# Kernel optimization log

Hardware: AMD Instinct MI355X
Metric: run time of the kernel (lower is better)

Reference implementation:

```python
import jax, jax.numpy as jnp
import numpy as np

N_NODES = 8192
N_EDGES = 131072  # avg degree 16
SD = 64   # state_dim == message_dim (required by readout input size)
MD = 64
H = 128   # hidden_unit_message_dim
HR = 128  # hidden_unit_readout_dim


def setup_inputs() -> dict:
    rng = np.random.default_rng(0)
    # distinct nonzero positions of J (COO), emulating torch.nonzero(J)
    flat = rng.choice(N_NODES * N_NODES, size=N_EDGES, replace=False)
    row = jnp.asarray(flat // N_NODES, dtype=jnp.int32)
    col = jnp.asarray(flat % N_NODES, dtype=jnp.int32)
    jvals = jnp.asarray(rng.normal(size=N_EDGES).astype(np.float32))  # J[row, col]
    b = jnp.asarray(rng.normal(size=N_NODES).astype(np.float32))     # unused by forward (as in source)

    key = jax.random.key(0)
    ks = jax.random.split(key, 12)
    p = lambda k, shape: 0.1 * jax.random.normal(k, shape, dtype=jnp.float32)
    return dict(
        jvals=jvals, b=b, row=row, col=col,
        conv_W=p(ks[0], (2, H, H)),          # GatedGraphConv per-layer weight
        gru_wi=p(ks[1], (3 * H, H)),          # GRUCell input weights (torch layout [3h,h])
        gru_wh=p(ks[2], (3 * H, H)),
        gru_bi=jnp.zeros((3 * H,), jnp.float32),
        gru_bh=jnp.zeros((3 * H,), jnp.float32),
        mp_W1=p(ks[3], (H, H)),  mp_b1=jnp.zeros((H,), jnp.float32),
        mp_W2=p(ks[4], (H, H)),  mp_b2=jnp.zeros((H,), jnp.float32),
        mp_W3=p(ks[5], (H, MD)), mp_b3=jnp.zeros((MD,), jnp.float32),
        ro_W1=p(ks[6], (SD, HR)), ro_b1=jnp.zeros((HR,), jnp.float32),
        ro_W2=p(ks[7], (HR, HR)), ro_b2=jnp.zeros((HR,), jnp.float32),
        ro_W3=p(ks[8], (HR, 2)),  ro_b3=jnp.zeros((2,), jnp.float32),
    )


def _ggnn_forward(jvals, b, row, col, conv_W, gru_wi, gru_wh, gru_bi, gru_bh,
                  mp_W1, mp_b1, mp_W2, mp_b2, mp_W3, mp_b3,
                  ro_W1, ro_b1, ro_W2, ro_b2, ro_W3, ro_b3):
    n_nodes = b.shape[0]
    n_edges = row.shape[0]
    n_tot = n_nodes + n_edges  # variable nodes + factor nodes

    # initial node states padded to hidden dim H (GatedGraphConv zero-pads input)
    x = jnp.zeros((n_tot, H), dtype=jvals.dtype)
    x = x.at[n_nodes:, 0].set(1.0).at[n_nodes:, 1].set(jvals)

    # bipartite factor-graph edges: factor e <-> row[e], factor e <-> col[e]
    fac = n_nodes + jnp.arange(n_edges, dtype=row.dtype)
    src = jnp.concatenate([fac, row, fac, col])
    dst = jnp.concatenate([row, fac, col, fac])

    # GatedGraphConv: 2 layers of (linear -> add-aggregate -> GRUCell)
    for l in range(2):
        m = x @ conv_W[l]                                   # [n_tot, H]
        agg = jax.ops.segment_sum(m[src], dst, num_segments=n_tot)
        gi = agg @ gru_wi.T + gru_bi                        # [n_tot, 3H]
        gh = x @ gru_wh.T + gru_bh
        i_r, i_z, i_n = jnp.split(gi, 3, axis=1)
        h_r, h_z, h_n = jnp.split(gh, 3, axis=1)
        r = jax.nn.sigmoid(i_r + h_r)
        z = jax.nn.sigmoid(i_z + h_z)
        n = jnp.tanh(i_n + r * h_n)
        x = (1.0 - z) * n + z * x

    # message MLP on factor-node states -> per-edge messages [n_edges, MD]
    xf = x[n_nodes:]
    hm = jax.nn.relu(xf @ mp_W1 + mp_b1)
    hm = jax.nn.relu(hm @ mp_W2 + mp_b2)
    msgs = hm @ mp_W3 + mp_b3

    # Special3dSpmm with b = ones: per-dim sparse row sums == segment_sum by row
    node_msgs = jax.ops.segment_sum(msgs, row, num_segments=n_nodes)  # [n_nodes, MD]

    hr = jax.nn.relu(node_msgs @ ro_W1 + ro_b1)
    hr = jax.nn.relu(hr @ ro_W2 + ro_b2)
    logits = hr @ ro_W3 + ro_b3
    return jax.nn.softmax(logits, axis=1)  # [n_nodes, 2]


def reference(jvals, b, row, col, conv_W, gru_wi, gru_wh, gru_bi, gru_bh,
              mp_W1, mp_b1, mp_W2, mp_b2, mp_W3, mp_b3,
              ro_W1, ro_b1, ro_W2, ro_b2, ro_W3, ro_b3):
    return _ggnn_forward(jvals, b, row, col, conv_W, gru_wi, gru_wh, gru_bi, gru_bh,
                         mp_W1, mp_b1, mp_W2, mp_b2, mp_W3, mp_b3,
                         ro_W1, ro_b1, ro_W2, ro_b2, ro_W3, ro_b3)
```

## Files before the change

### kernel.cpp

```cpp
#include <hip/hip_runtime.h>
#include <hip/hip_bf16.h>
#include <cstdint>

#define N_NODES 8192
#define N_EDGES 131072
#define NTOT 139264
#define H 128

typedef __attribute__((ext_vector_type(8))) short short8;
typedef __attribute__((ext_vector_type(4))) float floatx4;

__device__ __forceinline__ ushort f2bf(float f) {
    union { float f; uint32_t u; } v; v.f = f;
    uint32_t r = v.u + 0x7fffu + ((v.u >> 16) & 1u);
    return (ushort)(r >> 16);
}
__device__ __forceinline__ float bf2f(ushort u) {
    union { uint32_t u; float f; } v; v.u = ((uint32_t)u) << 16;
    return v.f;
}
__device__ __forceinline__ float bflo(uint u) { union { uint32_t u; float f; } v; v.u = u << 16; return v.f; }
__device__ __forceinline__ float bfhi(uint u) { union { uint32_t u; float f; } v; v.u = u & 0xffff0000u; return v.f; }
__device__ __forceinline__ uint packbf(float a, float b) { return (uint)f2bf(a) | ((uint)f2bf(b) << 16); }

__device__ __forceinline__ float fsig(float x) { return __builtin_amdgcn_rcpf(1.f + __expf(-x)); }
__device__ __forceinline__ float ftanh(float x) { return fmaf(2.f, fsig(2.f * x), -1.f); }

__device__ __forceinline__ short8 lds_load8(const ushort* p) {
    union { short8 s; uint2 u[2]; } r;
    r.u[0] = *(const uint2*)p;
    r.u[1] = *(const uint2*)(p + 4);
    return r.s;
}
__device__ __forceinline__ short8 glb_load8(const ushort* p) {
    union { short8 s; uint4 u; } r;
    r.u = *(const uint4*)p;
    return r.s;
}
__device__ __forceinline__ floatx4 mfma16(short8 a, short8 b, floatx4 c) {
    return __builtin_amdgcn_mfma_f32_16x16x32_bf16(a, b, c, 0, 0, 0);
}

__global__ __launch_bounds__(256) void k_setup(
    const float* __restrict__ convW, const float* __restrict__ wi, const float* __restrict__ wh,
    const float* __restrict__ m1, const float* __restrict__ m2, const float* __restrict__ m3,
    const float* __restrict__ r1, const float* __restrict__ r2,
    ushort* __restrict__ W, ushort* __restrict__ Wci,
    float* __restrict__ wh01, float* __restrict__ wci01)
{
    int idx = blockIdx.x * 256 + threadIdx.x;
    if (idx < 196608) {
        if (idx < 32768) { W[idx] = 0; return; }
        float v;
        if (idx < 81920)       v = wi[idx - 32768];
        else if (idx < 131072) v = wh[idx - 81920];
        else if (idx < 147456) { int t = idx - 131072; int n = t >> 7, k = t & 127; v = m1[k * 128 + n]; }
        else if (idx < 163840) { int t = idx - 147456; int n = t >> 7, k = t & 127; v = m2[k * 128 + n]; }
        else if (idx < 172032) { int t = idx - 163840; int n = t >> 7, k = t & 127; v = m3[k * 64 + n];  }
        else if (idx < 180224) { int t = idx - 172032; int n = t >> 6, k = t & 63;  v = r1[k * 128 + n]; }
        else                   { int t = idx - 180224; int n = t >> 7, k = t & 127; v = r2[k * 128 + n]; }
        W[idx] = f2bf(v);
    } else if (idx < 245760) {
        int t = idx - 196608;
        int n = t >> 7, k = t & 127;
        const float* wc = convW + 16384 + k * 128;
        const float* wr = wi + n * 128;
        float s = 0.f;
        #pragma unroll 8
        for (int j = 0; j < 128; ++j) s = fmaf(wc[j], wr[j], s);
        Wci[t] = f2bf(s);
    } else if (idx < 246528) {
        int n = idx - 245760;
        wh01[n] = wh[(n >> 1) * 128 + (n & 1)];
    } else if (idx < 247296) {
        int m = idx - 246528;
        int c = m >> 1, wsel = m & 1;
        const float* wc = convW + wsel * 128;
        const float* wr = wi + c * 128;
        float s = 0.f;
        #pragma unroll 8
        for (int j = 0; j < 128; ++j) s = fmaf(wc[j], wr[j], s);
        wci01[m] = s;
    }
}

__global__ __launch_bounds__(256) void k_zero_deg(int* __restrict__ deg, int* __restrict__ deg2) {
    int i = blockIdx.x * 256 + threadIdx.x;
    if (i < 8192) { deg[i] = 0; deg2[i] = 0; }
}

__global__ __launch_bounds__(256) void k_deg_count(const int* __restrict__ row, const int* __restrict__ col,
                                                   int* __restrict__ deg, int* __restrict__ deg2) {
    int e = blockIdx.x * 256 + threadIdx.x;
    atomicAdd(&deg[row[e]], 1);
    atomicAdd(&deg[col[e]], 1);
    atomicAdd(&deg2[row[e]], 1);
}

__global__ __launch_bounds__(256) void k_scan(const int* __restrict__ deg, int* __restrict__ start, int* __restrict__ cur,
                                              const int* __restrict__ deg2, int* __restrict__ start2, int* __restrict__ cur2) {
    __shared__ int s1[256], s2[256];
    int tid = threadIdx.x, base = tid * 32;
    int a = 0, b = 0;
    for (int i = 0; i < 32; ++i) { a += deg[base + i]; b += deg2[base + i]; }
    s1[tid] = a; s2[tid] = b;
    __syncthreads();
    if (tid == 0) {
        int acc = 0, acc2 = 0;
        for (int i = 0; i < 256; ++i) {
            int t = s1[i]; s1[i] = acc; acc += t;
            int u = s2[i]; s2[i] = acc2; acc2 += u;
        }
    }
    __syncthreads();
    int off = s1[tid], off2 = s2[tid];
    for (int i = 0; i < 32; ++i) {
        start[base + i] = off;  cur[base + i] = off;   off += deg[base + i];
        start2[base + i] = off2; cur2[base + i] = off2; off2 += deg2[base + i];
    }
}

__global__ __launch_bounds__(256) void k_fill(const int* __restrict__ row, const int* __restrict__ col,
                                              int* __restrict__ cur, int* __restrict__ cur2,
                                              int* __restrict__ list, int* __restrict__ list2) {
    int e = blockIdx.x * 256 + threadIdx.x;
    int p = atomicAdd(&cur[row[e]], 1);  list[p] = e;
    int q = atomicAdd(&cur[col[e]], 1);  list[q] = e;
    int r2 = atomicAdd(&cur2[row[e]], 1); list2[r2] = e;
}

#define SORT_BUF 256
__global__ __launch_bounds__(256) void k_sort(
    const int* __restrict__ start, const int* __restrict__ deg,
    const int* __restrict__ start2, const int* __restrict__ deg2,
    int* __restrict__ list, int* __restrict__ list2,
    const float* __restrict__ jvals, float* __restrict__ sj)
{
    __shared__ int bufU[4][SORT_BUF];
    __shared__ int bufS[4][SORT_BUF];
    const int wv = threadIdx.x >> 6, lane = threadIdx.x & 63;
    const int task = blockIdx.x * 4 + wv;
    const bool second = task >= 8192;
    const int node = second ? task - 8192 : task;
    const int s = second ? start2[node] : start[node];
    const int d = second ? deg2[node] : deg[node];
    int* L = second ? list2 : list;
    int* BU = bufU[wv];
    int* BS = bufS[wv];

    for (int i = lane; i < d && i < SORT_BUF; i += 64) BU[i] = L[s + i];
    __syncthreads();
    if (d <= SORT_BUF) {
        for (int i = lane; i < d; i += 64) {
            int v = BU[i];
            int rank = 0;
            for (int j = 0; j < d; ++j)
                rank += (BU[j] < v) || (BU[j] == v && j < i);
            L[s + rank] = v;
            BS[rank] = v;
        }
    } else if (lane == 0) {
        for (int a = 1; a < d; ++a) {
            int v = L[s + a]; int b = a - 1;
            while (b >= 0 && L[s + b] > v) { L[s + b + 1] = L[s + b]; --b; }
            L[s + b + 1] = v;
        }
    }
    __syncthreads();
    if (!second) {
        float a = 0.f;
        if (d <= SORT_BUF) {
            for (int i = lane; i < d; i += 64) a += jvals[BS[i]];
        } else if (lane == 0) {
            for (int i = 0; i < d; ++i) a += jvals[L[s + i]];
        }
        for (int off = 32; off; off >>= 1) a += __shfl_down(a, off);
        if (lane == 0) sj[node] = a;
    }
}

__global__ __launch_bounds__(256) void k_l1_fac(
    const float* __restrict__ jvals, const float* __restrict__ wh01,
    const float* __restrict__ bi, const float* __restrict__ bh, ushort* __restrict__ X1)
{
    int idx = blockIdx.x * 256 + threadIdx.x;
    int e = idx >> 6, cp = idx & 63;
    float jv = jvals[e];
    float res[2];
    #pragma unroll
    for (int t = 0; t < 2; ++t) {
        int c = 2 * cp + t;
        float ghr = fmaf(jv, wh01[c * 2 + 1], wh01[c * 2]) + bh[c];
        float ghz = fmaf(jv, wh01[(128 + c) * 2 + 1], wh01[(128 + c) * 2]) + bh[128 + c];
        float ghn = fmaf(jv, wh01[(256 + c) * 2 + 1], wh01[(256 + c) * 2]) + bh[256 + c];
        float r = fsig(bi[c] + ghr);
        float z = fsig(bi[128 + c] + ghz);
        float nn = ftanh(fmaf(r, ghn, bi[256 + c]));
        float x0 = (c == 0) ? 1.f : (c == 1 ? jv : 0.f);
        res[t] = (1.f - z) * nn + z * x0;
    }
    *(uint*)(X1 + (size_t)(N_NODES + e) * H + 2 * cp) = packbf(res[0], res[1]);
}

__global__ __launch_bounds__(256) void k_l1_nodes(
    const int* __restrict__ deg, const float* __restrict__ sj, const float* __restrict__ wci01,
    const float* __restrict__ bi, const float* __restrict__ bh, ushort* __restrict__ X1)
{
    int idx = blockIdx.x * 256 + threadIdx.x;
    int n = idx >> 6, cp = idx & 63;
    float d = (float)deg[n], s = sj[n];
    float res[2];
    #pragma unroll
    for (int t = 0; t < 2; ++t) {
        int c = 2 * cp + t;
        float gir = fmaf(s, wci01[c * 2 + 1], fmaf(d, wci01[c * 2], bi[c]));
        float giz = fmaf(s, wci01[(128 + c) * 2 + 1], fmaf(d, wci01[(128 + c) * 2], bi[128 + c]));
        float gin = fmaf(s, wci01[(256 + c) * 2 + 1], fmaf(d, wci01[(256 + c) * 2], bi[256 + c]));
        float r = fsig(gir + bh[c]);
        float z = fsig(giz + bh[128 + c]);
        float nn = ftanh(fmaf(r, bh[256 + c], gin));
        res[t] = (1.f - z) * nn;
    }
    *(uint*)(X1 + (size_t)n * H + 2 * cp) = packbf(res[0], res[1]);
}

__global__ __launch_bounds__(256) void k_agg_nodes(uint* __restrict__ Pn, const uint* __restrict__ X,
                                                   const int* __restrict__ start, const int* __restrict__ deg,
                                                   const int* __restrict__ list) {
    int node = blockIdx.x * 4 + (threadIdx.x >> 6);
    int lane = threadIdx.x & 63;
    int s = start[node], d = deg[node];
    float a0 = 0.f, b0 = 0.f, a1 = 0.f, b1 = 0.f;
    int i = 0;
    for (; i + 1 < d; i += 2) {
        uint v0 = X[(size_t)(N_NODES + list[s + i]) * 64 + lane];
        uint v1 = X[(size_t)(N_NODES + list[s + i + 1]) * 64 + lane];
        a0 += bflo(v0); b0 += bfhi(v0);
        a1 += bflo(v1); b1 += bfhi(v1);
    }
    if (i < d) {
        uint v0 = X[(size_t)(N_NODES + list[s + i]) * 64 + lane];
        a0 += bflo(v0); b0 += bfhi(v0);
    }
    Pn[(size_t)node * 64 + lane] = packbf(a0 + a1, b0 + b1);
}

__global__ __launch_bounds__(256) void k_nm_gather(float* __restrict__ nm, const ushort* __restrict__ msgs,
                                                   const int* __restrict__ start2, const int* __restrict__ deg2,
                                                   const int* __restrict__ list2) {
    int node = blockIdx.x * 4 + (threadIdx.x >> 6);
    int lane = threadIdx.x & 63;
    int s = start2[node], d = deg2[node];
    float a0 = 0.f, a1 = 0.f;
    int i = 0;
    for (; i + 1 < d; i += 2) {
        a0 += bf2f(msgs[(size_t)list2[s + i] * 64 + lane]);
        a1 += bf2f(msgs[(size_t)list2[s + i + 1] * 64 + lane]);
    }
    if (i < d) a0 += bf2f(msgs[(size_t)list2[s + i] * 64 + lane]);
    nm[(size_t)node * 64 + lane] = a0 + a1;
}

__global__ __launch_bounds__(256) void k_logits(const ushort* __restrict__ hr2, const float* __restrict__ W3,
                                                const float* __restrict__ b3, float* __restrict__ out) {
    int r = blockIdx.x * 4 + (threadIdx.x >> 6);
    int lane = threadIdx.x & 63;
    float l0 = 0.f, l1 = 0.f;
    for (int k = lane; k < H; k += 64) {
        float hv = bf2f(hr2[(size_t)r * H + k]);
        l0 = fmaf(hv, W3[k * 2 + 0], l0);
        l1 = fmaf(hv, W3[k * 2 + 1], l1);
    }
    for (int off = 32; off; off >>= 1) { l0 += __shfl_down(l0, off); l1 += __shfl_down(l1, off); }
    if (lane == 0) {
        l0 += b3[0]; l1 += b3[1];
        float mx = fmaxf(l0, l1);
        float e0 = __expf(l0 - mx), e1 = __expf(l1 - mx), s = e0 + e1;
        out[r * 2 + 0] = e0 / s;
        out[r * 2 + 1] = e1 / s;
    }
}

template<int BN, bool AF32, bool RELU, bool OUTF32>
__global__ __launch_bounds__(256) void k_gemm2(
    const void* __restrict__ Aptr, const ushort* __restrict__ Bt,
    const float* __restrict__ bias, void* __restrict__ Cptr, int K, int lda)
{
    constexpr int BM = 128, LK = 136;
    constexpr int MI = (BN == 128) ? 4 : 2;
    constexpr int NI = 4;
    __shared__ ushort As[BM * LK];
    __shared__ ushort Bs[BN * LK];
    const int tid = threadIdx.x;
    const size_t row0 = (size_t)blockIdx.x * BM;
    const int kpc = K >> 3;

    if (AF32) {
        const float* A = (const float*)Aptr;
        for (int id = tid; id < BM * kpc; id += 256) {
            int m = id / kpc, kc = id - m * kpc;
            float4 v0 = *(const float4*)(A + (row0 + m) * lda + kc * 8);
            float4 v1 = *(const float4*)(A + (row0 + m) * lda + kc * 8 + 4);
            uint4 u;
            u.x = packbf(v0.x, v0.y); u.y = packbf(v0.z, v0.w);
            u.z = packbf(v1.x, v1.y); u.w = packbf(v1.z, v1.w);
            *(uint4*)&As[m * LK + kc * 8] = u;
        }
    } else {
        const ushort* A = (const ushort*)Aptr;
        for (int id = tid; id < BM * kpc; id += 256) {
            int m = id / kpc, kc = id - m * kpc;
            *(uint4*)&As[m * LK + kc * 8] = *(const uint4*)(A + (row0 + m) * (size_t)lda + kc * 8);
        }
    }
    for (int id = tid; id < BN * kpc; id += 256) {
        int slot = id / kpc, kc = id - slot * kpc;
        int gcol = (slot & ~63) + 4 * (slot & 15) + ((slot >> 4) & 3);
        *(uint4*)&Bs[slot * LK + kc * 8] = *(const uint4*)(Bt + (size_t)gcol * K + kc * 8);
    }
    __syncthreads();

    const int w = tid >> 6, lane = tid & 63, quad = lane >> 4, l15 = lane & 15;
    const int wr = (BN == 128) ? (w >> 1) * 64 : w * 32;
    const int wc = (BN == 128) ? (w & 1) * 64 : 0;

    floatx4 acc[MI][NI];
    #pragma unroll
    for (int i = 0; i < MI; ++i)
        #pragma unroll
        for (int j = 0; j < NI; ++j) acc[i][j] = (floatx4)0.f;

    for (int k0 = 0; k0 < K; k0 += 32) {
        short8 a[MI], b[NI];
        #pragma unroll
        for (int mi = 0; mi < MI; ++mi) a[mi] = lds_load8(&As[(wr + mi * 16 + l15) * LK + k0 + quad * 8]);
        #pragma unroll
        for (int ni = 0; ni < NI; ++ni) b[ni] = lds_load8(&Bs[(wc + ni * 16 + l15) * LK + k0 + quad * 8]);
        #pragma unroll
        for (int mi = 0; mi < MI; ++mi)
            #pragma unroll
            for (int ni = 0; ni < NI; ++ni)
                acc[mi][ni] = mfma16(a[mi], b[ni], acc[mi][ni]);
    }

    float bv[NI];
    #pragma unroll
    for (int ni = 0; ni < NI; ++ni) bv[ni] = bias ? bias[wc + 4 * l15 + ni] : 0.f;
    #pragma unroll
    for (int mi = 0; mi < MI; ++mi) {
        #pragma unroll
        for (int reg = 0; reg < 4; ++reg) {
            size_t r = row0 + wr + mi * 16 + quad * 4 + reg;
            float v[NI];
            #pragma unroll
            for (int ni = 0; ni < NI; ++ni) {
                v[ni] = acc[mi][ni][reg] + bv[ni];
                if (RELU) v[ni] = fmaxf(v[ni], 0.f);
            }
            if (OUTF32) {
                float4 o = make_float4(v[0], v[1], v[2], v[3]);
                *(float4*)((float*)Cptr + r * BN + wc + 4 * l15) = o;
            } else {
                uint2 o = make_uint2(packbf(v[0], v[1]), packbf(v[2], v[3]));
                *(uint2*)((ushort*)Cptr + r * BN + wc + 4 * l15) = o;
            }
        }
    }
}

__global__ __launch_bounds__(512, 4) void k_gru6(
    const ushort* __restrict__ Pn, const ushort* __restrict__ Xin, ushort* __restrict__ Xout,
    const int* __restrict__ row, const int* __restrict__ col,
    const ushort* __restrict__ WCI, const ushort* __restrict__ WH,
    const float* __restrict__ bi, const float* __restrict__ bh)
{
    constexpr int LK = 136;
    __shared__ ushort Ws[3 * 64 * LK];
    const int tid = threadIdx.x;
    const int c0 = blockIdx.x * 64;
    const size_t brow0 = (size_t)blockIdx.y * 128;
    const bool isFac = blockIdx.y >= (N_NODES / 128);
    const int w = tid >> 6, lane = tid & 63, quad = lane >> 4, l15 = lane & 15;
    const int ch = w & 1;
    const size_t row0 = brow0 + (w >> 1) * 32;
    const int cb = c0 + ch * 32;

    int srcR[2], srcC[2];
    if (isFac) {
        #pragma unroll
        for (int mi = 0; mi < 2; ++mi) {
            int e = (int)(row0 + mi * 16 + l15) - N_NODES;
            srcR[mi] = row[e];
            srcC[mi] = col[e];
        }
    }

    floatx4 accR[2][2], accZ[2][2], accI[2][2], accHN[2][2];
    #pragma unroll
    for (int i = 0; i < 2; ++i)
        #pragma unroll
        for (int j = 0; j < 2; ++j) {
            accR[i][j] = (floatx4)0.f; accZ[i][j] = (floatx4)0.f;
            accI[i][j] = (floatx4)0.f; accHN[i][j] = (floatx4)0.f;
        }

    #pragma unroll
    for (int h = 0; h < 2; ++h) {
        if (h) __syncthreads();
        const ushort* Wsrc = h ? WH : WCI;
        for (int id = tid; id < 3072; id += 512) {
            int kc = id & 15, slot = (id >> 4) & 63, s = id >> 10;
            int w32 = slot & 31;
            int gcol = c0 + (slot >> 5) * 32 + 2 * (w32 & 15) + (w32 >> 4);
            *(uint4*)&Ws[(s * 64 + slot) * LK + kc * 8] =
                *(const uint4*)(Wsrc + (size_t)(s * 128 + gcol) * 128 + kc * 8);
        }
        __syncthreads();
        if (h == 0) {
            if (isFac) {
                #pragma unroll
                for (int k4 = 0; k4 < 4; ++k4) {
                    const int k0 = k4 * 32;
                    short8 ar[2], ac[2];
                    #pragma unroll
                    for (int mi = 0; mi < 2; ++mi) {
                        ar[mi] = glb_load8(Xin + (size_t)srcR[mi] * H + k0 + quad * 8);
                        ac[mi] = glb_load8(Xin + (size_t)srcC[mi] * H + k0 + quad * 8);
                    }
                    #pragma unroll
                    for (int s = 0; s < 3; ++s) {
                        short8 b[2];
                        #pragma unroll
                        for (int ni = 0; ni < 2; ++ni)
                            b[ni] = lds_load8(&Ws[(s * 64 + ch * 32 + ni * 16 + l15) * LK + k0 + quad * 8]);
                        #pragma unroll
                        for (int mi = 0; mi < 2; ++mi)
                            #pragma unroll
                            for (int ni = 0; ni < 2; ++ni) {
                                if (s == 0) { accR[mi][ni] = mfma16(ar[mi], b[ni], accR[mi][ni]);
                                              accR[mi][ni] = mfma16(ac[mi], b[ni], accR[mi][ni]); }
                                else if (s == 1) { accZ[mi][ni] = mfma16(ar[mi], b[ni], accZ[mi][ni]);
                                                   accZ[mi][ni] = mfma16(ac[mi], b[ni], accZ[mi][ni]); }
                                else { accI[mi][ni] = mfma16(ar[mi], b[ni], accI[mi][ni]);
                                       accI[mi][ni] = mfma16(ac[mi], b[ni], accI[mi][ni]); }
                            }
                    }
                }
            } else {
                #pragma unroll
                for (int k4 = 0; k4 < 4; ++k4) {
                    const int k0 = k4 * 32;
                    short8 a[2];
                    #pragma unroll
                    for (int mi = 0; mi < 2; ++mi)
                        a[mi] = glb_load8(Pn + (row0 + mi * 16 + l15) * H + k0 + quad * 8);
                    #pragma unroll
                    for (int s = 0; s < 3; ++s) {
                        short8 b[2];
                        #pragma unroll
                        for (int ni = 0; ni < 2; ++ni)
                            b[ni] = lds_load8(&Ws[(s * 64 + ch * 32 + ni * 16 + l15) * LK + k0 + quad * 8]);
                        #pragma unroll
                        for (int mi = 0; mi < 2; ++mi)
                            #pragma unroll
                            for (int ni = 0; ni < 2; ++ni) {
                                if (s == 0)      accR[mi][ni] = mfma16(a[mi], b[ni], accR[mi][ni]);
                                else if (s == 1) accZ[mi][ni] = mfma16(a[mi], b[ni], accZ[mi][ni]);
                                else             accI[mi][ni] = mfma16(a[mi], b[ni], accI[mi][ni]);
                            }
                    }
                }
            }
        } else {
            #pragma unroll
            for (int k4 = 0; k4 < 4; ++k4) {
                const int k0 = k4 * 32;
                short8 a[2];
                #pragma unroll
                for (int mi = 0; mi < 2; ++mi)
                    a[mi] = glb_load8(Xin + (row0 + mi * 16 + l15) * H + k0 + quad * 8);
                #pragma unroll
                for (int s = 0; s < 3; ++s) {
                    short8 b[2];
                    #pragma unroll
                    for (int ni = 0; ni < 2; ++ni)
                        b[ni] = lds_load8(&Ws[(s * 64 + ch * 32 + ni * 16 + l15) * LK + k0 + quad * 8]);
                    #pragma unroll
                    for (int mi = 0; mi < 2; ++mi)
                        #pragma unroll
                        for (int ni = 0; ni < 2; ++ni) {
                            if (s == 0)      accR[mi][ni] = mfma16(a[mi], b[ni], accR[mi][ni]);
                            else if (s == 1) accZ[mi][ni] = mfma16(a[mi], b[ni], accZ[mi][ni]);
                            else             accHN[mi][ni] = mfma16(a[mi], b[ni], accHN[mi][ni]);
                        }
                }
            }
        }
    }

    const int ce = cb + 2 * l15;
    float bir[2], biz[2], bin_[2], bhr[2], bhz[2], bhn[2];
    #pragma unroll
    for (int ni = 0; ni < 2; ++ni) {
        bir[ni] = bi[ce + ni]; biz[ni] = bi[128 + ce + ni]; bin_[ni] = bi[256 + ce + ni];
        bhr[ni] = bh[ce + ni]; bhz[ni] = bh[128 + ce + ni]; bhn[ni] = bh[256 + ce + ni];
    }
    #pragma unroll
    for (int mi = 0; mi < 2; ++mi)
        #pragma unroll
        for (int reg = 0; reg < 4; ++reg) {
            size_t r = row0 + mi * 16 + quad * 4 + reg;
            uint xo = *(const uint*)(Xin + r * H + ce);
            float xold[2] = { bflo(xo), bfhi(xo) };
            float res[2];
            #pragma unroll
            for (int ni = 0; ni < 2; ++ni) {
                float rs = accR[mi][ni][reg] + bir[ni] + bhr[ni];
                float zs = accZ[mi][ni][reg] + biz[ni] + bhz[ni];
                float rr = fsig(rs);
                float zz = fsig(zs);
                float nn = ftanh(accI[mi][ni][reg] + bin_[ni] + rr * (accHN[mi][ni][reg] + bhn[ni]));
                res[ni] = (1.f - zz) * nn + zz * xold[ni];
            }
            *(uint*)(Xout + r * H + ce) = packbf(res[0], res[1]);
        }
}

__global__ __launch_bounds__(256, 3) void k_mlp(
    const ushort* __restrict__ Xf, const ushort* __restrict__ W1, const ushort* __restrict__ W2,
    const ushort* __restrict__ W3, const float* __restrict__ b1, const float* __restrict__ b2,
    const float* __restrict__ b3, ushort* __restrict__ msgs)
{
    constexpr int LK = 132;
    __shared__ ushort T[128 * LK];
    __shared__ ushort Wv[64 * LK];
    const int tid = threadIdx.x;
    const size_t row0 = (size_t)blockIdx.x * 128;
    const int w = tid >> 6, lane = tid & 63, quad = lane >> 4, l15 = lane & 15;
    const int wr = w * 32;

    for (int id = tid; id < 2048; id += 256) {
        int m = id >> 4, kc = (id & 15) * 8;
        *(uint4*)&T[m * LK + kc] = *(const uint4*)(Xf + (row0 + m) * H + kc);
    }

    #pragma unroll
    for (int stage = 0; stage < 3; ++stage) {
        const ushort* Wsrc = (stage == 0) ? W1 : (stage == 1) ? W2 : W3;
        const float* bias = (stage == 0) ? b1 : (stage == 1) ? b2 : b3;
        const int NCG = (stage == 2) ? 1 : 2;
        floatx4 acc[2][2][4];
        #pragma unroll
        for (int c = 0; c < 2; ++c)
            #pragma unroll
            for (int i = 0; i < 2; ++i)
                #pragma unroll
                for (int j = 0; j < 4; ++j) acc[c][i][j] = (floatx4)0.f;

        for (int cg = 0; cg < NCG; ++cg) {
            __syncthreads();
            for (int id = tid; id < 1024; id += 256) {
                int slot = id >> 4, kc = (id & 15) * 8;
                int gcol = cg * 64 + 4 * (slot & 15) + (slot >> 4);
                *(uint4*)&Wv[slot * LK + kc] = *(const uint4*)(Wsrc + (size_t)gcol * 128 + kc);
            }
            __syncthreads();
            for (int k0 = 0; k0 < 128; k0 += 32) {
                short8 a[2], b[4];
                #pragma unroll
                for (int mi = 0; mi < 2; ++mi)
                    a[mi] = lds_load8(&T[(wr + mi * 16 + l15) * LK + k0 + quad * 8]);
                #pragma unroll
                for (int ni = 0; ni < 4; ++ni)
                    b[ni] = lds_load8(&Wv[(ni * 16 + l15) * LK + k0 + quad * 8]);
                #pragma unroll
                for (int mi = 0; mi < 2; ++mi)
                    #pragma unroll
                    for (int ni = 0; ni < 4; ++ni)
                        acc[cg][mi][ni] = mfma16(a[mi], b[ni], acc[cg][mi][ni]);
            }
        }
        __syncthreads();

        if (stage < 2) {
            #pragma unroll
            for (int cg = 0; cg < 2; ++cg) {
                float bv[4];
                #pragma unroll
                for (int ni = 0; ni < 4; ++ni) bv[ni] = bias[cg * 64 + 4 * l15 + ni];
                #pragma unroll
                for (int mi = 0; mi < 2; ++mi)
                    #pragma unroll
                    for (int reg = 0; reg < 4; ++reg) {
                        int r = wr + mi * 16 + quad * 4 + reg;
                        float v[4];
                        #pragma unroll
                        for (int ni = 0; ni < 4; ++ni)
                            v[ni] = fmaxf(acc[cg][mi][ni][reg] + bv[ni], 0.f);
                        uint2 o = make_uint2(packbf(v[0], v[1]), packbf(v[2], v[3]));
                        *(uint2*)&T[r * LK + cg * 64 + 4 * l15] = o;
                    }
            }
            __syncthreads();
        } else {
            float bv[4];
            #pragma unroll
            for (int ni = 0; ni < 4; ++ni) bv[ni] = bias[4 * l15 + ni];
            #pragma unroll
            for (int mi = 0; mi < 2; ++mi)
                #pragma unroll
                for (int reg = 0; reg < 4; ++reg) {
                    size_t r = row0 + wr + mi * 16 + quad * 4 + reg;
                    float v[4];
                    #pragma unroll
                    for (int ni = 0; ni < 4; ++ni) v[ni] = acc[0][mi][ni][reg] + bv[ni];
                    uint2 o = make_uint2(packbf(v[0], v[1]), packbf(v[2], v[3]));
                    *(uint2*)(msgs + r * 64 + 4 * l15) = o;
                }
        }
    }
}

extern "C" void kernel_launch(void* const* d_in, const int* in_sizes, int n_in,
                              void* d_out, int out_size, void* d_ws, size_t ws_size,
                              hipStream_t stream) {
    (void)in_sizes; (void)n_in; (void)out_size;
    const float* jvals  = (const float*)d_in[0];
    const int*   row    = (const int*)d_in[2];
    const int*   col    = (const int*)d_in[3];
    const float* conv_W = (const float*)d_in[4];
    const float* gru_wi = (const float*)d_in[5];
    const float* gru_wh = (const float*)d_in[6];
    const float* gru_bi = (const float*)d_in[7];
    const float* gru_bh = (const float*)d_in[8];
    const float* mp_W1  = (const float*)d_in[9];
    const float* mp_b1  = (const float*)d_in[10];
    const float* mp_W2  = (const float*)d_in[11];
    const float* mp_b2  = (const float*)d_in[12];
    const float* mp_W3  = (const float*)d_in[13];
    const float* mp_b3  = (const float*)d_in[14];
    const float* ro_b1  = (const float*)d_in[16];
    const float* ro_b2  = (const float*)d_in[18];
    const float* ro_W3  = (const float*)d_in[19];
    const float* ro_b3  = (const float*)d_in[20];

    constexpr size_t OFF_XB  = 35651584ull;
    constexpr size_t OFF_P   = 71303168ull;
    constexpr size_t OFF_W   = 106954752ull;
    constexpr size_t OFF_WCI = 107347968ull;
    constexpr size_t OFF_NM  = 107544576ull;
    constexpr size_t OFF_HR1 = 109641728ull;
    constexpr size_t OFF_HR2 = 111738880ull;
    constexpr size_t OFF_CSR = 113836032ull;
    constexpr size_t OFF_L1  = 114032640ull;
    constexpr size_t OFF_L2  = 115081216ull;
    constexpr size_t OFF_SJ  = 115605504ull;
    constexpr size_t OFF_WH01  = 115638272ull;
    constexpr size_t OFF_WCI01 = 115641344ull;
    constexpr size_t WS_NEED = 115644416ull;
    if (ws_size < WS_NEED) return;

    char* ws = (char*)d_ws;
    ushort* X2   = (ushort*)ws;
    ushort* X1   = (ushort*)(ws + OFF_XB);
    ushort* Pn   = (ushort*)(ws + OFF_P);
    ushort* msgs = (ushort*)(ws + OFF_P);
    ushort* Wb   = (ushort*)(ws + OFF_W);
    ushort* Wci  = (ushort*)(ws + OFF_WCI);
    float*  nm   = (float*)(ws + OFF_NM);
    ushort* hr1  = (ushort*)(ws + OFF_HR1);
    ushort* hr2  = (ushort*)(ws + OFF_HR2);
    int* deg    = (int*)(ws + OFF_CSR);
    int* start  = deg + 8192;
    int* cur    = deg + 16384;
    int* deg2   = deg + 24576;
    int* start2 = deg + 32768;
    int* cur2   = deg + 40960;
    int* list   = (int*)(ws + OFF_L1);
    int* list2  = (int*)(ws + OFF_L2);
    float* sj    = (float*)(ws + OFF_SJ);
    float* wh01  = (float*)(ws + OFF_WH01);
    float* wci01 = (float*)(ws + OFF_WCI01);

    dim3 blk(256);

    k_setup<<<966, blk, 0, stream>>>(conv_W, gru_wi, gru_wh, mp_W1, mp_W2, mp_W3,
                                     (const float*)d_in[15], (const float*)d_in[17],
                                     Wb, Wci, wh01, wci01);
    k_zero_deg<<<32, blk, 0, stream>>>(deg, deg2);
    k_deg_count<<<N_EDGES / 256, blk, 0, stream>>>(row, col, deg, deg2);
    k_scan<<<1, blk, 0, stream>>>(deg, start, cur, deg2, start2, cur2);
    k_fill<<<N_EDGES / 256, blk, 0, stream>>>(row, col, cur, cur2, list, list2);
    k_sort<<<4096, blk, 0, stream>>>(start, deg, start2, deg2, list, list2, jvals, sj);

    k_l1_fac<<<N_EDGES * 64 / 256, blk, 0, stream>>>(jvals, wh01, gru_bi, gru_bh, X1);
    k_l1_nodes<<<N_NODES * 64 / 256, blk, 0, stream>>>(deg, sj, wci01, gru_bi, gru_bh, X1);

    k_agg_nodes<<<N_NODES / 4, blk, 0, stream>>>((uint*)Pn, (const uint*)X1, start, deg, list);
    k_gru6<<<dim3(2, NTOT / 128), dim3(512), 0, stream>>>(Pn, X1, X2, row, col,
        Wci, Wb + 81920, gru_bi, gru_bh);

    k_mlp<<<N_EDGES / 128, blk, 0, stream>>>(
        X2 + (size_t)N_NODES * H, Wb + 131072, Wb + 147456, Wb + 163840,
        mp_b1, mp_b2, mp_b3, msgs);

    k_nm_gather<<<N_NODES / 4, blk, 0, stream>>>(nm, msgs, start2, deg2, list2);

    k_gemm2<128, true, true, false><<<N_NODES / 128, blk, 0, stream>>>(
        nm, Wb + 172032, ro_b1, hr1, 64, 64);
    k_gemm2<128, false, true, false><<<N_NODES / 128, blk, 0, stream>>>(
        hr1, Wb + 180224, ro_b2, hr2, 128, 128);
    k_logits<<<N_NODES / 4, blk, 0, stream>>>(hr2, ro_W3, ro_b3, (float*)d_out);
}
```

Measured before the change: 357.3 us.

## Process both column halves per GRU block and stage output through LDS

The layer-2 GRU kernel now has each block loop over both 64-column halves of the output, instead of launching two blocks per row tile. The gathered row/col indices are loaded once per block, and the activation rows are re-read while still likely resident in cache. Results are written to a shared-memory tile first and then stored to global memory as coalesced 16-byte rows, replacing the scattered 4-byte stores. The cost is half as many blocks, more barriers, and weights reloaded into LDS four times per block instead of twice.

```diff
diff --git a/kernel.cpp b/kernel.cpp
--- a/kernel.cpp
+++ b/kernel.cpp
@@ -368,7 +368,7 @@
     }
 }
 
-__global__ __launch_bounds__(512, 4) void k_gru6(
+__global__ __launch_bounds__(512, 4) void k_gru7(
     const ushort* __restrict__ Pn, const ushort* __restrict__ Xin, ushort* __restrict__ Xout,
     const int* __restrict__ row, const int* __restrict__ col,
     const ushort* __restrict__ WCI, const ushort* __restrict__ WH,
@@ -376,14 +376,14 @@
 {
     constexpr int LK = 136;
     __shared__ ushort Ws[3 * 64 * LK];
+    uint* tile32 = (uint*)Ws;
     const int tid = threadIdx.x;
-    const int c0 = blockIdx.x * 64;
-    const size_t brow0 = (size_t)blockIdx.y * 128;
-    const bool isFac = blockIdx.y >= (N_NODES / 128);
+    const size_t brow0 = (size_t)blockIdx.x * 128;
+    const bool isFac = blockIdx.x >= (N_NODES / 128);
     const int w = tid >> 6, lane = tid & 63, quad = lane >> 4, l15 = lane & 15;
     const int ch = w & 1;
-    const size_t row0 = brow0 + (w >> 1) * 32;
-    const int cb = c0 + ch * 32;
+    const int wg = w >> 1;
+    const size_t row0 = brow0 + wg * 32;
 
     int srcR[2], srcC[2];
     if (isFac) {
@@ -395,55 +395,82 @@
         }
     }
 
-    floatx4 accR[2][2], accZ[2][2], accI[2][2], accHN[2][2];
-    #pragma unroll
-    for (int i = 0; i < 2; ++i)
-        #pragma unroll
-        for (int j = 0; j < 2; ++j) {
-            accR[i][j] = (floatx4)0.f; accZ[i][j] = (floatx4)0.f;
-            accI[i][j] = (floatx4)0.f; accHN[i][j] = (floatx4)0.f;
-        }
-
-    #pragma unroll
-    for (int h = 0; h < 2; ++h) {
-        if (h) __syncthreads();
-        const ushort* Wsrc = h ? WH : WCI;
-        for (int id = tid; id < 3072; id += 512) {
-            int kc = id & 15, slot = (id >> 4) & 63, s = id >> 10;
-            int w32 = slot & 31;
-            int gcol = c0 + (slot >> 5) * 32 + 2 * (w32 & 15) + (w32 >> 4);
-            *(uint4*)&Ws[(s * 64 + slot) * LK + kc * 8] =
-                *(const uint4*)(Wsrc + (size_t)(s * 128 + gcol) * 128 + kc * 8);
-        }
-        __syncthreads();
-        if (h == 0) {
-            if (isFac) {
-                #pragma unroll
-                for (int k4 = 0; k4 < 4; ++k4) {
-                    const int k0 = k4 * 32;
-                    short8 ar[2], ac[2];
+    for (int p = 0; p < 2; ++p) {
+        const int c0 = p * 64;
+        floatx4 accR[2][2], accZ[2][2], accI[2][2], accHN[2][2];
+        #pragma unroll
+        for (int i = 0; i < 2; ++i)
+            #pragma unroll
+            for (int j = 0; j < 2; ++j) {
+                accR[i][j] = (floatx4)0.f; accZ[i][j] = (floatx4)0.f;
+                accI[i][j] = (floatx4)0.f; accHN[i][j] = (floatx4)0.f;
+            }
+
+        #pragma unroll
+        for (int h = 0; h < 2; ++h) {
+            __syncthreads();
+            const ushort* Wsrc = h ? WH : WCI;
+            for (int id = tid; id < 3072; id += 512) {
+                int kc = id & 15, slot = (id >> 4) & 63, s = id >> 10;
+                int w32 = slot & 31;
+                int gcol = c0 + (slot >> 5) * 32 + 2 * (w32 & 15) + (w32 >> 4);
+                *(uint4*)&Ws[(s * 64 + slot) * LK + kc * 8] =
+                    *(const uint4*)(Wsrc + (size_t)(s * 128 + gcol) * 128 + kc * 8);
+            }
+            __syncthreads();
+            if (h == 0) {
+                if (isFac) {
                     #pragma unroll
-                    for (int mi = 0; mi < 2; ++mi) {
-                        ar[mi] = glb_load8(Xin + (size_t)srcR[mi] * H + k0 + quad * 8);
-                        ac[mi] = glb_load8(Xin + (size_t)srcC[mi] * H + k0 + quad * 8);
+                    for (int k4 = 0; k4 < 4; ++k4) {
+                        const int k0 = k4 * 32;
+                        short8 ar[2], ac[2];
+                        #pragma unroll
+                        for (int mi = 0; mi < 2; ++mi) {
+                            ar[mi] = glb_load8(Xin + (size_t)srcR[mi] * H + k0 + quad * 8);
+                            ac[mi] = glb_load8(Xin + (size_t)srcC[mi] * H + k0 + quad * 8);
+                        }
+                        #pragma unroll
+                        for (int s = 0; s < 3; ++s) {
+                            short8 b[2];
+                            #pragma unroll
+                            for (int ni = 0; ni < 2; ++ni)
+                                b[ni] = lds_load8(&Ws[(s * 64 + ch * 32 + ni * 16 + l15) * LK + k0 + quad * 8]);
+                            #pragma unroll
+                            for (int mi = 0; mi < 2; ++mi)
+                                #pragma unroll
+                                for (int ni = 0; ni < 2; ++ni) {
+                                    if (s == 0) { accR[mi][ni] = mfma16(ar[mi], b[ni], accR[mi][ni]);
+                                                  accR[mi][ni] = mfma16(ac[mi], b[ni], accR[mi][ni]); }
+                                    else if (s == 1) { accZ[mi][ni] = mfma16(ar[mi], b[ni], accZ[mi][ni]);
+                                                       accZ[mi][ni] = mfma16(ac[mi], b[ni], accZ[mi][ni]); }
+                                    else { accI[mi][ni] = mfma16(ar[mi], b[ni], accI[mi][ni]);
+                                           accI[mi][ni] = mfma16(ac[mi], b[ni], accI[mi][ni]); }
+                                }
+                        }
                     }
+                } else {
                     #pragma unroll
-                    for (int s = 0; s < 3; ++s) {
-                        short8 b[2];
-                        #pragma unroll
-                        for (int ni = 0; ni < 2; ++ni)
-                            b[ni] = lds_load8(&Ws[(s * 64 + ch * 32 + ni * 16 + l15) * LK + k0 + quad * 8]);
+                    for (int k4 = 0; k4 < 4; ++k4) {
+                        const int k0 = k4 * 32;
+                        short8 a[2];
                         #pragma unroll
                         for (int mi = 0; mi < 2; ++mi)
+                            a[mi] = glb_load8(Pn + (row0 + mi * 16 + l15) * H + k0 + quad * 8);
+                        #pragma unroll
+                        for (int s = 0; s < 3; ++s) {
+                            short8 b[2];
                             #pragma unroll
-                            for (int ni = 0; ni < 2; ++ni) {
-                                if (s == 0) { accR[mi][ni] = mfma16(ar[mi], b[ni], accR[mi][ni]);
-                                              accR[mi][ni] = mfma16(ac[mi], b[ni], accR[mi][ni]); }
-                                else if (s == 1) { accZ[mi][ni] = mfma16(ar[mi], b[ni], accZ[mi][ni]);
-                                                   accZ[mi][ni] = mfma16(ac[mi], b[ni], accZ[mi][ni]); }
-                                else { accI[mi][ni] = mfma16(ar[mi], b[ni], accI[mi][ni]);
-                                       accI[mi][ni] = mfma16(ac[mi], b[ni], accI[mi][ni]); }
-                            }
+                            for (int ni = 0; ni < 2; ++ni)
+                                b[ni] = lds_load8(&Ws[(s * 64 + ch * 32 + ni * 16 + l15) * LK + k0 + quad * 8]);
+                            #pragma unroll
+                            for (int mi = 0; mi < 2; ++mi)
+                                #pragma unroll
+                                for (int ni = 0; ni < 2; ++ni) {
+                                    if (s == 0)      accR[mi][ni] = mfma16(a[mi], b[ni], accR[mi][ni]);
+                                    else if (s == 1) accZ[mi][ni] = mfma16(a[mi], b[ni], accZ[mi][ni]);
+                                    else             accI[mi][ni] = mfma16(a[mi], b[ni], accI[mi][ni]);
+                                }
+                        }
                     }
                 }
             } else {
@@ -453,7 +480,7 @@
                     short8 a[2];
                     #pragma unroll
                     for (int mi = 0; mi < 2; ++mi)
-                        a[mi] = glb_load8(Pn + (row0 + mi * 16 + l15) * H + k0 + quad * 8);
+                        a[mi] = glb_load8(Xin + (row0 + mi * 16 + l15) * H + k0 + quad * 8);
                     #pragma unroll
                     for (int s = 0; s < 3; ++s) {
                         short8 b[2];
@@ -466,64 +493,56 @@
                             for (int ni = 0; ni < 2; ++ni) {
                                 if (s == 0)      accR[mi][ni] = mfma16(a[mi], b[ni], accR[mi][ni]);
                                 else if (s == 1) accZ[mi][ni] = mfma16(a[mi], b[ni], accZ[mi][ni]);
-                                else             accI[mi][ni] = mfma16(a[mi], b[ni], accI[mi][ni]);
+                                else             accHN[mi][ni] = mfma16(a[mi], b[ni], accHN[mi][ni]);
                             }
                     }
                 }
             }
-        } else {
-            #pragma unroll
-            for (int k4 = 0; k4 < 4; ++k4) {
-                const int k0 = k4 * 32;
-                short8 a[2];
-                #pragma unroll
-                for (int mi = 0; mi < 2; ++mi)
-                    a[mi] = glb_load8(Xin + (row0 + mi * 16 + l15) * H + k0 + quad * 8);
-                #pragma unroll
-                for (int s = 0; s < 3; ++s) {
-                    short8 b[2];
-                    #pragma unroll
-                    for (int ni = 0; ni < 2; ++ni)
-                        b[ni] = lds_load8(&Ws[(s * 64 + ch * 32 + ni * 16 + l15) * LK + k0 + quad * 8]);
-                    #pragma unroll
-                    for (int mi = 0; mi < 2; ++mi)
-                        #pragma unroll
-                        for (int ni = 0; ni < 2; ++ni) {
-                            if (s == 0)      accR[mi][ni] = mfma16(a[mi], b[ni], accR[mi][ni]);
-                            else if (s == 1) accZ[mi][ni] = mfma16(a[mi], b[ni], accZ[mi][ni]);
-                            else             accHN[mi][ni] = mfma16(a[mi], b[ni], accHN[mi][ni]);
-                        }
+        }
+
+        const int cb = c0 + ch * 32;
+        const int ce = cb + 2 * l15;
+        float bir[2], biz[2], bin_[2], bhr[2], bhz[2], bhn[2];
+        #pragma unroll
+        for (int ni = 0; ni < 2; ++ni) {
+            bir[ni] = bi[ce + ni]; biz[ni] = bi[128 + ce + ni]; bin_[ni] = bi[256 + ce + ni];
+            bhr[ni] = bh[ce + ni]; bhz[ni] = bh[128 + ce + ni]; bhn[ni] = bh[256 + ce + ni];
+        }
+        uint resu[2][4];
+        #pragma unroll
+        for (int mi = 0; mi < 2; ++mi)
+            #pragma unroll
+            for (int reg = 0; reg < 4; ++reg) {
+                size_t r = row0 + mi * 16 + quad * 4 + reg;
+                uint xo = *(const uint*)(Xin + r * H + ce);
+                float xold[2] = { bflo(xo), bfhi(xo) };
+                float res[2];
+                #pragma unroll
+                for (int ni = 0; ni < 2; ++ni) {
+                    float rs = accR[mi][ni][reg] + bir[ni] + bhr[ni];
+                    float zs = accZ[mi][ni][reg] + biz[ni] + bhz[ni];
+                    float rr = fsig(rs);
+                    float zz = fsig(zs);
+                    float nn = ftanh(accI[mi][ni][reg] + bin_[ni] + rr * (accHN[mi][ni][reg] + bhn[ni]));
+                    res[ni] = (1.f - zz) * nn + zz * xold[ni];
                 }
-            }
-        }
-    }
-
-    const int ce = cb + 2 * l15;
-    float bir[2], biz[2], bin_[2], bhr[2], bhz[2], bhn[2];
-    #pragma unroll
-    for (int ni = 0; ni < 2; ++ni) {
-        bir[ni] = bi[ce + ni]; biz[ni] = bi[128 + ce + ni]; bin_[ni] = bi[256 + ce + ni];
-        bhr[ni] = bh[ce + ni]; bhz[ni] = bh[128 + ce + ni]; bhn[ni] = bh[256 + ce + ni];
-    }
-    #pragma unroll
-    for (int mi = 0; mi < 2; ++mi)
-        #pragma unroll
-        for (int reg = 0; reg < 4; ++reg) {
-            size_t r = row0 + mi * 16 + quad * 4 + reg;
-            uint xo = *(const uint*)(Xin + r * H + ce);
-            float xold[2] = { bflo(xo), bfhi(xo) };
-            float res[2];
-            #pragma unroll
-            for (int ni = 0; ni < 2; ++ni) {
-                float rs = accR[mi][ni][reg] + bir[ni] + bhr[ni];
-                float zs = accZ[mi][ni][reg] + biz[ni] + bhz[ni];
-                float rr = fsig(rs);
-                float zz = fsig(zs);
-                float nn = ftanh(accI[mi][ni][reg] + bin_[ni] + rr * (accHN[mi][ni][reg] + bhn[ni]));
-                res[ni] = (1.f - zz) * nn + zz * xold[ni];
-            }
-            *(uint*)(Xout + r * H + ce) = packbf(res[0], res[1]);
-        }
+                resu[mi][reg] = packbf(res[0], res[1]);
+            }
+        __syncthreads();
+        #pragma unroll
+        for (int mi = 0; mi < 2; ++mi)
+            #pragma unroll
+            for (int reg = 0; reg < 4; ++reg) {
+                int rl = wg * 32 + mi * 16 + quad * 4 + reg;
+                tile32[rl * 32 + ch * 16 + l15] = resu[mi][reg];
+            }
+        __syncthreads();
+        for (int id = tid; id < 1024; id += 512) {
+            int r = id >> 3, c16 = id & 7;
+            *(uint4*)(Xout + (brow0 + r) * H + c0 + c16 * 8) =
+                *(const uint4*)((const ushort*)tile32 + r * 64 + c16 * 8);
+        }
+    }
 }
 
 __global__ __launch_bounds__(256, 3) void k_mlp(
@@ -697,7 +716,7 @@
     k_l1_nodes<<<N_NODES * 64 / 256, blk, 0, stream>>>(deg, sj, wci01, gru_bi, gru_bh, X1);
 
     k_agg_nodes<<<N_NODES / 4, blk, 0, stream>>>((uint*)Pn, (const uint*)X1, start, deg, list);
-    k_gru6<<<dim3(2, NTOT / 128), dim3(512), 0, stream>>>(Pn, X1, X2, row, col,
+    k_gru7<<<NTOT / 128, dim3(512), 0, stream>>>(Pn, X1, X2, row, col,
         Wci, Wb + 81920, gru_bi, gru_bh);
 
     k_mlp<<<N_EDGES / 128, blk, 0, stream>>>(
```

Result: slower. 399.9 us (+11.9%).
